# Kernel tuning notes

Hardware: AMD Instinct MI355X
Metric: run time of the kernel (lower is better)

The kernel has to match this reference:

```python
import jax, jax.numpy as jnp
import numpy as np

D = 128
H = 4
DK = D // H


def _spmm(row, col, val, x, n):
    # sparse.mm(adj, x) with adj in COO form: out[row] += val * x[col]
    return jax.ops.segment_sum(val[:, None] * x[col], row, num_segments=n)


def _arrg(h, a1_w, a1_b, a2_w, a2_b):
    return jax.nn.leaky_relu(h @ a1_w + a1_b, negative_slope=0.01) @ a2_w + a2_b


def _cross_attn(x, q_x, q_w, k_w, v_w):
    n, d = x.shape
    m = q_x.shape[0]
    q = (q_x @ q_w).reshape(m, H, DK).transpose(1, 0, 2)   # [H, Q, dk]
    k = (x @ k_w).reshape(n, H, DK).transpose(1, 0, 2)     # [H, N, dk]
    v = (q_x @ v_w).reshape(m, H, DK).transpose(1, 0, 2)   # [H, Q, dk]
    s = jnp.einsum('hnd,hqd->hnq', k, q) / jnp.sqrt(jnp.float32(DK))
    w = jax.nn.softmax(s, axis=-1)                          # softmax over queries
    out = jnp.einsum('hnq,hqd->hnd', w, v).transpose(1, 0, 2).reshape(n, d)
    return out + x


def setup_inputs() -> dict:
    key = jax.random.key(0)
    ks = iter(jax.random.split(key, 64))
    nrm = lambda shape, s=0.05: jax.random.normal(next(ks), shape, jnp.float32) * s
    inp = {}
    inp['trans_w'] = nrm((1, D)); inp['trans_b'] = nrm((D,))
    inp['g_w'] = nrm((D, D));     inp['g_b'] = nrm((D,))
    inp['qg_w'] = nrm((D, D));    inp['qg_b'] = nrm((D,))
    inp['q_w'] = nrm((D, D)); inp['k_w'] = nrm((D, D)); inp['v_w'] = nrm((D, D))
    inp['a1_w'] = nrm((D, 2 * D)); inp['a1_b'] = nrm((2 * D,))
    inp['a2_w'] = nrm((2 * D, D)); inp['a2_b'] = nrm((D,))
    inp['x0'] = jax.random.normal(next(ks), (25000,), jnp.float32)
    inp['q0'] = jax.random.normal(next(ks), (100,), jnp.float32)
    for i in (1, 2, 3):
        inp[f'xin{i}'] = jax.random.normal(next(ks), (25000,), jnp.float32)
        inp[f'qin{i}'] = jax.random.normal(next(ks), (100,), jnp.float32)
    n_sizes = {1: 50000, 2: 75000, 3: 100000}
    q_sizes = {1: 200, 2: 300, 3: 400}
    for i in (1, 2, 3):
        e = 16 * n_sizes[i]
        inp[f'aval{i}'] = jax.random.uniform(next(ks), (e,), jnp.float32)
        inp[f'arow{i}'] = jax.random.randint(next(ks), (e,), 0, n_sizes[i], jnp.int64)
        inp[f'acol{i}'] = jax.random.randint(next(ks), (e,), 0, n_sizes[i], jnp.int64)
        qe = 16 * q_sizes[i]
        inp[f'qval{i}'] = jax.random.uniform(next(ks), (qe,), jnp.float32)
        inp[f'qrow{i}'] = jax.random.randint(next(ks), (qe,), 0, q_sizes[i], jnp.int64)
        inp[f'qcol{i}'] = jax.random.randint(next(ks), (qe,), 0, q_sizes[i], jnp.int64)
    return inp


def reference(trans_w, trans_b, g_w, g_b, qg_w, qg_b, q_w, k_w, v_w,
              a1_w, a1_b, a2_w, a2_b,
              x0, q0, xin1, xin2, xin3, qin1, qin2, qin3,
              aval1, aval2, aval3, qval1, qval2, qval3,
              arow1, acol1, arow2, acol2, arow3, acol3,
              qrow1, qcol1, qrow2, qcol2, qrow3, qcol3):
    trans = lambda v: v[:, None] @ trans_w + trans_b
    x = trans(x0)
    qx = trans(q0)
    steps = [
        (xin1, qin1, arow1, acol1, aval1, qrow1, qcol1, qval1, 50000, 200),
        (xin2, qin2, arow2, acol2, aval2, qrow2, qcol2, qval2, 75000, 300),
        (xin3, qin3, arow3, acol3, aval3, qrow3, qcol3, qval3, 100000, 400),
    ]
    for xin, qin, ar, ac, av, qr, qc, qv, n, m in steps:
        x = jnp.concatenate([x, trans(xin)], axis=0)
        qx = jnp.concatenate([qx, trans(qin)], axis=0)
        x = _spmm(ar, ac, av, x @ g_w + g_b, n)
        qx = _spmm(qr, qc, qv, qx @ qg_w + qg_b, m)
        x = _arrg(x, a1_w, a1_b, a2_w, a2_b)
        qx = _arrg(qx, a1_w, a1_b, a2_w, a2_b)
        x = _cross_attn(x, qx, q_w, k_w, v_w)
    return (x, qx)
```

## Files before the change

kernel.cpp:

```cpp
#include <hip/hip_runtime.h>

typedef unsigned short u16;
typedef __attribute__((ext_vector_type(8))) short bf16x8;
typedef __attribute__((ext_vector_type(4))) float f32x4;
typedef __attribute__((ext_vector_type(2))) unsigned u32x2;

__device__ __forceinline__ float b2f(u16 v) {
    return __uint_as_float(((unsigned)v) << 16);
}
__device__ __forceinline__ u16 f2b(float x) {
    unsigned u = __float_as_uint(x);
    unsigned r = u + 0x7FFFu + ((u >> 16) & 1u);
    return (u16)(r >> 16);
}
__device__ __forceinline__ float4 load_bf4(const u16* p) {
    ushort4 q = *(const ushort4*)p;
    float4 f;
    f.x = b2f(q.x); f.y = b2f(q.y); f.z = b2f(q.z); f.w = b2f(q.w);
    return f;
}
__device__ __forceinline__ float4 in4(const void* p, long off, bool bf) {
    if (bf) return load_bf4((const u16*)p + off);
    return *(const float4*)((const float*)p + off);
}
__device__ __forceinline__ float in1(const void* p, long off, bool bf) {
    if (bf) return b2f(((const u16*)p)[off]);
    return ((const float*)p)[off];
}
__device__ __forceinline__ int inIdx(const void* p, long i, bool i64) {
    return ((const int*)p)[i64 ? 2 * i : i];
}

__global__ void sniff_kernel(const u16* __restrict__ x0bits, const int* __restrict__ arow,
                             int* __restrict__ flags) {
    if (threadIdx.x != 0 || blockIdx.x != 0) return;
    int plaus = 0;
    for (int i = 0; i < 256; ++i) {
        u16 v = x0bits[i];
        int e = (v >> 7) & 0xFF;
        if (v == 0 || (e >= 100 && e <= 135)) plaus++;
    }
    flags[0] = (plaus >= 200) ? 1 : 0;
    int nz = 0;
    for (int i = 1; i < 128; i += 2) nz += (arow[i] != 0);
    flags[1] = (nz == 0) ? 1 : 0;
}

__global__ void trans_kernel(const void* __restrict__ v, const void* __restrict__ tw,
                             const void* __restrict__ tb, float* __restrict__ out,
                             int rows, const int* __restrict__ flags) {
    const bool bf = flags[0] != 0;
    int t = blockIdx.x * blockDim.x + threadIdx.x;
    int c4 = (t & 31) * 4;
    int r = t >> 5;
    if (r >= rows) return;
    float vv = in1(v, r, bf);
    float4 w4 = in4(tw, c4, bf);
    float4 b4 = in4(tb, c4, bf);
    float4 o;
    o.x = vv * w4.x + b4.x; o.y = vv * w4.y + b4.y;
    o.z = vv * w4.z + b4.z; o.w = vv * w4.w + b4.w;
    *(float4*)(out + (size_t)r * 128 + c4) = o;
}

__global__ void wprep_kernel(const void* __restrict__ src, u16* __restrict__ dst,
                             int K, int N, const int* __restrict__ flags) {
    const bool bf = flags[0] != 0;
    int idx = blockIdx.x * blockDim.x + threadIdx.x;
    if (idx >= K * N) return;
    int j = idx & 7, lane = (idx >> 3) & 63, t = idx >> 9;
    int KC = K >> 5;
    int kc = t % KC, ct = t / KC;
    int k = kc * 32 + (lane >> 4) * 8 + j;
    int nn = ct * 16 + (lane & 15);
    dst[idx] = f2b(in1(src, (long)k * N + nn, bf));
}

template<int KTOT, int NOUT, bool LEAKY, typename AT, typename CT>
__launch_bounds__(256)
__global__ void gemm_mfma_kernel(const AT* __restrict__ A, const u16* __restrict__ Wf,
                                 const void* __restrict__ bias, CT* __restrict__ C,
                                 int n, const int* __restrict__ flags) {
    constexpr int KC = KTOT / 32;
    constexpr int NT = NOUT / 16;
    __shared__ u16 wlds[KTOT * NOUT];
    {
        const int4* srcw = (const int4*)Wf;
        int4* dstw = (int4*)wlds;
        constexpr int NV = KTOT * NOUT * 2 / 16;
#pragma unroll
        for (int i = 0; i < NV / 256; ++i)
            dstw[i * 256 + threadIdx.x] = srcw[i * 256 + threadIdx.x];
    }
    __syncthreads();
    const bool bf = flags[0] != 0;
    const int lane = threadIdx.x & 63;
    const int wave = threadIdx.x >> 6;
    const int quad = lane >> 4, col = lane & 15;
    const int rbase = (blockIdx.x * 4 + wave) * 16;
    if (rbase >= n) return;
    int node = rbase + col; if (node >= n) node = n - 1;
    f32x4 acc[NT];
#pragma unroll
    for (int ct = 0; ct < NT; ++ct) acc[ct] = (f32x4){0.f, 0.f, 0.f, 0.f};
#pragma unroll
    for (int kc = 0; kc < KC; ++kc) {
        bf16x8 af;
        if constexpr (sizeof(AT) == 2) {
            af = *(const bf16x8*)((const u16*)A + (size_t)node * KTOT + kc * 32 + quad * 8);
        } else {
            const float* ap = (const float*)A + (size_t)node * KTOT + kc * 32 + quad * 8;
            float4 a0 = *(const float4*)ap;
            float4 a1 = *(const float4*)(ap + 4);
            af[0] = (short)f2b(a0.x); af[1] = (short)f2b(a0.y);
            af[2] = (short)f2b(a0.z); af[3] = (short)f2b(a0.w);
            af[4] = (short)f2b(a1.x); af[5] = (short)f2b(a1.y);
            af[6] = (short)f2b(a1.z); af[7] = (short)f2b(a1.w);
        }
#pragma unroll
        for (int ct = 0; ct < NT; ++ct) {
            bf16x8 wf = *(const bf16x8*)(wlds + (((ct * KC + kc) * 64 + lane) * 8));
            acc[ct] = __builtin_amdgcn_mfma_f32_16x16x32_bf16(af, wf, acc[ct], 0, 0, 0);
        }
    }
#pragma unroll
    for (int ct = 0; ct < NT; ++ct) {
        int colg = ct * 16 + col;
        float b = bias ? in1(bias, colg, bf) : 0.f;
#pragma unroll
        for (int r = 0; r < 4; ++r) {
            int row = rbase + quad * 4 + r;
            if (row >= n) continue;
            float v = acc[ct][r] + b;
            if (LEAKY) v = v > 0.f ? v : 0.01f * v;
            if constexpr (sizeof(CT) == 2) C[(size_t)row * NOUT + colg] = (CT)f2b(v);
            else                           C[(size_t)row * NOUT + colg] = (CT)v;
        }
    }
}

__launch_bounds__(256)
__global__ void gemm_qv_kernel(const float* __restrict__ A, const u16* __restrict__ Wfq,
                               const u16* __restrict__ Wfv, float* __restrict__ Cq,
                               float* __restrict__ Cv, int n) {
    __shared__ u16 wldsq[128 * 128];
    __shared__ u16 wldsv[128 * 128];
    {
        const int4* sq = (const int4*)Wfq;
        const int4* sv = (const int4*)Wfv;
        int4* dq = (int4*)wldsq;
        int4* dv = (int4*)wldsv;
#pragma unroll
        for (int i = 0; i < 8; ++i) {
            dq[i * 256 + threadIdx.x] = sq[i * 256 + threadIdx.x];
            dv[i * 256 + threadIdx.x] = sv[i * 256 + threadIdx.x];
        }
    }
    __syncthreads();
    const int lane = threadIdx.x & 63;
    const int wave = threadIdx.x >> 6;
    const int quad = lane >> 4, col = lane & 15;
    const int rbase = (blockIdx.x * 4 + wave) * 16;
    if (rbase >= n) return;
    int node = rbase + col; if (node >= n) node = n - 1;
    f32x4 accq[8], accv[8];
#pragma unroll
    for (int ct = 0; ct < 8; ++ct) {
        accq[ct] = (f32x4){0.f, 0.f, 0.f, 0.f};
        accv[ct] = (f32x4){0.f, 0.f, 0.f, 0.f};
    }
#pragma unroll
    for (int kc = 0; kc < 4; ++kc) {
        const float* ap = A + (size_t)node * 128 + kc * 32 + quad * 8;
        float4 a0 = *(const float4*)ap;
        float4 a1 = *(const float4*)(ap + 4);
        bf16x8 af;
        af[0] = (short)f2b(a0.x); af[1] = (short)f2b(a0.y);
        af[2] = (short)f2b(a0.z); af[3] = (short)f2b(a0.w);
        af[4] = (short)f2b(a1.x); af[5] = (short)f2b(a1.y);
        af[6] = (short)f2b(a1.z); af[7] = (short)f2b(a1.w);
#pragma unroll
        for (int ct = 0; ct < 8; ++ct) {
            bf16x8 wq = *(const bf16x8*)(wldsq + (((ct * 4 + kc) * 64 + lane) * 8));
            bf16x8 wv = *(const bf16x8*)(wldsv + (((ct * 4 + kc) * 64 + lane) * 8));
            accq[ct] = __builtin_amdgcn_mfma_f32_16x16x32_bf16(af, wq, accq[ct], 0, 0, 0);
            accv[ct] = __builtin_amdgcn_mfma_f32_16x16x32_bf16(af, wv, accv[ct], 0, 0, 0);
        }
    }
#pragma unroll
    for (int ct = 0; ct < 8; ++ct) {
        int colg = ct * 16 + col;
#pragma unroll
        for (int r = 0; r < 4; ++r) {
            int row = rbase + quad * 4 + r;
            if (row >= n) continue;
            Cq[(size_t)row * 128 + colg] = accq[ct][r];
            Cv[(size_t)row * 128 + colg] = accv[ct][r];
        }
    }
}

#define RSH 8
#define NBC_MAX 512
#define EPB 4096

__global__ void zero_int_kernel(int* __restrict__ p, int n) {
    int i = blockIdx.x * blockDim.x + threadIdx.x;
    if (i < n) p[i] = 0;
}

__global__ void bhist_kernel(const void* __restrict__ rows, int e, int* __restrict__ bcnt,
                             int nbc, const int* __restrict__ flags) {
    __shared__ int hist[NBC_MAX];
    const bool i64 = flags[1] != 0;
    for (int i = threadIdx.x; i < nbc; i += 256) hist[i] = 0;
    __syncthreads();
    int base = blockIdx.x * 8192;
    int end = base + 8192; if (end > e) end = e;
    for (int i = base + threadIdx.x; i < end; i += 256)
        atomicAdd(&hist[inIdx(rows, i, i64) >> RSH], 1);
    __syncthreads();
    for (int i = threadIdx.x; i < nbc; i += 256) {
        int c = hist[i];
        if (c) atomicAdd(&bcnt[i], c);
    }
}

__global__ void scanF_kernel(const int* __restrict__ bcnt, int nbc,
                             int* __restrict__ optr, int* __restrict__ ocur) {
    __shared__ int sc[NBC_MAX];
    const int tid = threadIdx.x;
    int v0 = (tid < nbc) ? bcnt[tid] : 0;
    int v1 = (tid + 256 < nbc) ? bcnt[tid + 256] : 0;
    sc[tid] = v0; sc[tid + 256] = v1;
    __syncthreads();
    for (int off = 1; off < NBC_MAX; off <<= 1) {
        int a = (tid >= off) ? sc[tid - off] : 0;
        int b = sc[tid + 256 - off];
        __syncthreads();
        sc[tid] += a;
        sc[tid + 256] += b;
        __syncthreads();
    }
    if (tid < nbc)       { int x = sc[tid] - v0;       optr[tid] = x;       ocur[tid] = x; }
    if (tid + 256 < nbc) { int x = sc[tid + 256] - v1; optr[tid + 256] = x; ocur[tid + 256] = x; }
}

__launch_bounds__(256)
__global__ void qbuild_kernel(const void* __restrict__ rows, const void* __restrict__ colsin,
                              const void* __restrict__ valsin, int e, int nrows,
                              int2* __restrict__ pack1, int* __restrict__ rowptr,
                              int* __restrict__ rowend, const int* __restrict__ flags) {
    __shared__ int hist[512], cur[512], sc[512];
    const bool bf = flags[0] != 0;
    const bool i64 = flags[1] != 0;
    const int tid = threadIdx.x;
    for (int i = tid; i < 512; i += 256) hist[i] = 0;
    __syncthreads();
    for (int i = tid; i < e; i += 256)
        atomicAdd(&hist[inIdx(rows, i, i64)], 1);
    __syncthreads();
    int v0 = hist[tid], v1 = hist[tid + 256];
    sc[tid] = v0; sc[tid + 256] = v1;
    __syncthreads();
    for (int off = 1; off < 512; off <<= 1) {
        int a = (tid >= off) ? sc[tid - off] : 0;
        int b = sc[tid + 256 - off];
        __syncthreads();
        sc[tid] += a;
        sc[tid + 256] += b;
        __syncthreads();
    }
    {
        int x = sc[tid] - v0;
        cur[tid] = x;
        if (tid < nrows) { rowptr[tid] = x; rowend[tid] = x + v0; }
        int x1 = sc[tid + 256] - v1;
        cur[tid + 256] = x1;
        if (tid + 256 < nrows) { rowptr[tid + 256] = x1; rowend[tid + 256] = x1 + v1; }
    }
    __syncthreads();
    for (int i = tid; i < e; i += 256) {
        int r = inIdx(rows, i, i64);
        int p = atomicAdd(&cur[r], 1);
        pack1[p] = (int2){inIdx(colsin, i, i64), __float_as_int(in1(valsin, i, bf))};
    }
}

__launch_bounds__(256)
__global__ void psort_kernel(const void* __restrict__ rows, const void* __restrict__ colsin,
                             const void* __restrict__ valsin, int e,
                             int* __restrict__ gcur, int2* __restrict__ pack0,
                             int nbc, const int* __restrict__ flags) {
    __shared__ int hist[NBC_MAX];
    __shared__ int scan[NBC_MAX];
    __shared__ int base[NBC_MAX];
    __shared__ int cur[NBC_MAX];
    __shared__ int2 stage[EPB];
    __shared__ u16 binof[EPB];
    const bool bf = flags[0] != 0;
    const bool i64 = flags[1] != 0;
    const int tid = threadIdx.x;
    const long s0 = (long)blockIdx.x * EPB;
    int cnt_e = e - (int)s0; if (cnt_e > EPB) cnt_e = EPB;

    for (int i = tid; i < NBC_MAX; i += 256) hist[i] = 0;
    __syncthreads();
    for (int j = tid; j < cnt_e; j += 256)
        atomicAdd(&hist[inIdx(rows, s0 + j, i64) >> RSH], 1);
    __syncthreads();
    for (int i = tid; i < NBC_MAX; i += 256) scan[i] = hist[i];
    __syncthreads();
    for (int off = 1; off < NBC_MAX; off <<= 1) {
        int a = (tid >= off) ? scan[tid - off] : 0;
        int c = scan[tid + 256 - off];
        __syncthreads();
        scan[tid] += a;
        scan[tid + 256] += c;
        __syncthreads();
    }
    for (int i = tid; i < nbc; i += 256) {
        int h = hist[i];
        cur[i] = scan[i] - h;
        base[i] = h ? atomicAdd(&gcur[i], h) : 0;
    }
    __syncthreads();
    for (int j = tid; j < cnt_e; j += 256) {
        int r = inIdx(rows, s0 + j, i64);
        int bin = r >> RSH;
        int p = atomicAdd(&cur[bin], 1);
        int2 pk;
        pk.x = ((r & ((1 << RSH) - 1)) << 20) | inIdx(colsin, s0 + j, i64);
        pk.y = __float_as_int(in1(valsin, s0 + j, bf));
        stage[p] = pk;
        binof[p] = (u16)bin;
    }
    __syncthreads();
    for (int j = tid; j < cnt_e; j += 256) {
        int bin = binof[j];
        int st = scan[bin] - hist[bin];
        pack0[base[bin] + (j - st)] = stage[j];
    }
}

__launch_bounds__(256)
__global__ void breorder256_kernel(const int2* __restrict__ pack0, const int* __restrict__ bptr,
                                   const int* __restrict__ bend, int2* __restrict__ pack1,
                                   int* __restrict__ rowptr, int* __restrict__ rowend, int n) {
    __shared__ int hist[256], scan[256], cur[256];
    const int b = blockIdx.x;
    const int s = bptr[b], e = bend[b];
    const int tid = threadIdx.x;
    hist[tid] = 0;
    __syncthreads();
    for (int i = s + tid; i < e; i += 256)
        atomicAdd(&hist[(unsigned)pack0[i].x >> 20], 1);
    __syncthreads();
    scan[tid] = hist[tid];
    __syncthreads();
    for (int off = 1; off < 256; off <<= 1) {
        int a = (tid >= off) ? scan[tid - off] : 0;
        __syncthreads();
        scan[tid] += a;
        __syncthreads();
    }
    int st = s + scan[tid] - hist[tid];
    cur[tid] = st;
    int rg = (b << RSH) + tid;
    if (rg < n) { rowptr[rg] = st; rowend[rg] = st + hist[tid]; }
    __syncthreads();
    for (int i = s + tid; i < e; i += 256) {
        int2 pk = pack0[i];
        int rl = (unsigned)pk.x >> 20;
        int p = atomicAdd(&cur[rl], 1);
        pack1[p] = (int2){pk.x & 0xFFFFF, pk.y};
    }
}

__device__ __forceinline__ void bffma8(float v, uint4 h, float* a) {
    a[0] += v * __uint_as_float(h.x << 16);
    a[1] += v * __uint_as_float(h.x & 0xFFFF0000u);
    a[2] += v * __uint_as_float(h.y << 16);
    a[3] += v * __uint_as_float(h.y & 0xFFFF0000u);
    a[4] += v * __uint_as_float(h.z << 16);
    a[5] += v * __uint_as_float(h.z & 0xFFFF0000u);
    a[6] += v * __uint_as_float(h.w << 16);
    a[7] += v * __uint_as_float(h.w & 0xFFFF0000u);
}
__global__ void spmm_kernel(const u16* __restrict__ H, const int* __restrict__ rowptr,
                            const int* __restrict__ rowend, const int2* __restrict__ pack,
                            u16* __restrict__ out, int n) {
    int w = threadIdx.x >> 6;
    int lane = threadIdx.x & 63;
    int r = blockIdx.x * 4 + w;
    if (r >= n) return;
    const int s16 = lane >> 4;
    const int l16 = lane & 15;
    int s = rowptr[r], e = rowend[r];
    float a[8] = {0.f, 0.f, 0.f, 0.f, 0.f, 0.f, 0.f, 0.f};
    int i = s + s16;
    for (; i + 12 < e; i += 16) {
        int2 p0 = pack[i], p1 = pack[i + 4], p2 = pack[i + 8], p3 = pack[i + 12];
        uint4 h0 = *(const uint4*)(H + (size_t)p0.x * 128 + l16 * 8);
        uint4 h1 = *(const uint4*)(H + (size_t)p1.x * 128 + l16 * 8);
        uint4 h2 = *(const uint4*)(H + (size_t)p2.x * 128 + l16 * 8);
        uint4 h3 = *(const uint4*)(H + (size_t)p3.x * 128 + l16 * 8);
        bffma8(__int_as_float(p0.y), h0, a);
        bffma8(__int_as_float(p1.y), h1, a);
        bffma8(__int_as_float(p2.y), h2, a);
        bffma8(__int_as_float(p3.y), h3, a);
    }
    for (; i < e; i += 4) {
        int2 p0 = pack[i];
        uint4 h0 = *(const uint4*)(H + (size_t)p0.x * 128 + l16 * 8);
        bffma8(__int_as_float(p0.y), h0, a);
    }
#pragma unroll
    for (int k = 0; k < 8; ++k) {
        a[k] += __shfl_xor(a[k], 16, 64);
        a[k] += __shfl_xor(a[k], 32, 64);
    }
    if (s16 == 0) {
        uint4 o;
        o.x = (unsigned)f2b(a[0]) | ((unsigned)f2b(a[1]) << 16);
        o.y = (unsigned)f2b(a[2]) | ((unsigned)f2b(a[3]) << 16);
        o.z = (unsigned)f2b(a[4]) | ((unsigned)f2b(a[5]) << 16);
        o.w = (unsigned)f2b(a[6]) | ((unsigned)f2b(a[7]) << 16);
        *(uint4*)(out + (size_t)r * 128 + l16 * 8) = o;
    }
}

__global__ void attn_prep_kernel(const float* __restrict__ Qq, const float* __restrict__ Qv,
                                 u16* __restrict__ Qf, u16* __restrict__ Vf,
                                 int m, int mt32) {
    int idx = blockIdx.x * blockDim.x + threadIdx.x;
    int total = 4 * mt32 * 1024;
    if (idx >= total) return;
    const int mt16 = mt32 * 2;
    const float scale = 0.17677669529663687f * 1.44269504088896340736f;
    {
        int j = idx & 7, lane = (idx >> 3) & 63;
        int t = idx >> 9;
        int h = t / mt16, qt = t - h * mt16;
        int dim = ((lane >> 4) & 3) * 8 + j;
        int query = qt * 16 + (lane & 15);
        Qf[idx] = (query < m) ? f2b(Qq[(size_t)query * 128 + h * 32 + dim] * scale) : (u16)0;
    }
    {
        int j = idx & 7, lane = (idx >> 3) & 63;
        int u = idx >> 9;
        int dh = u & 1, t = u >> 1;
        int h = t / mt32, qc = t - h * mt32;
        int query = qc * 32 + ((lane >> 4) & 3) * 8 + j;
        int dim = dh * 16 + (lane & 15);
        Vf[idx] = (query < m) ? f2b(Qv[(size_t)query * 128 + h * 32 + dim]) : (u16)0;
    }
}

__launch_bounds__(256)
__global__ void attn_mfma_kernel(const u16* __restrict__ Kb, const u16* __restrict__ Qf,
                                 const u16* __restrict__ Vf, float* __restrict__ X,
                                 int n, int m, int mt32, int pad) {
    __shared__ __align__(128) u16 Pbuf_all[4 * 1024];
    const int h = blockIdx.y;
    const int wave = threadIdx.x >> 6;
    const int lane = threadIdx.x & 63;
    const int nb = (blockIdx.x * 4 + wave) * 32;
    if (nb >= n) return;
    const int quad = lane >> 4, col = lane & 15;
    int node0 = nb + col;      if (node0 >= n) node0 = n - 1;
    int node1 = nb + 16 + col; if (node1 >= n) node1 = n - 1;
    bf16x8 kf0 = *(const bf16x8*)(Kb + (size_t)node0 * 128 + h * 32 + quad * 8);
    bf16x8 kf1 = *(const bf16x8*)(Kb + (size_t)node1 * 128 + h * 32 + quad * 8);
    f32x4 O00 = {0.f, 0.f, 0.f, 0.f}, O01 = {0.f, 0.f, 0.f, 0.f};
    f32x4 O10 = {0.f, 0.f, 0.f, 0.f}, O11 = {0.f, 0.f, 0.f, 0.f};
    const f32x4 zero = {0.f, 0.f, 0.f, 0.f};
    float Lp0[4] = {0.f, 0.f, 0.f, 0.f};
    float Lp1[4] = {0.f, 0.f, 0.f, 0.f};
    u16* Pw0 = Pbuf_all + wave * 1024;
    u16* Pw1 = Pw0 + 512;
    uint2* pw0[2]; uint2* pw1[2];
    pw0[0] = (uint2*)(Pw0 + col * 16 + quad * 4);
    pw0[1] = (uint2*)(Pw0 + 256 + col * 16 + quad * 4);
    pw1[0] = (uint2*)(Pw1 + col * 16 + quad * 4);
    pw1[1] = (uint2*)(Pw1 + 256 + col * 16 + quad * 4);
    const unsigned paddr0 = (unsigned)(uintptr_t)Pw0 + (unsigned)(quad * 256 + col * 8);
    const unsigned paddr1 = (unsigned)(uintptr_t)Pw1 + (unsigned)(quad * 256 + col * 8);
    const u16* Qbase = Qf + (size_t)h * (mt32 * 2) * 512;
    const u16* Vbase = Vf + (size_t)h * mt32 * 1024;
    for (int qc = 0; qc < mt32; ++qc) {
#pragma unroll
        for (int half = 0; half < 2; ++half) {
            bf16x8 qfr = *(const bf16x8*)(Qbase + (size_t)(qc * 2 + half) * 512 + lane * 8);
            f32x4 S0 = __builtin_amdgcn_mfma_f32_16x16x32_bf16(kf0, qfr, zero, 0, 0, 0);
            f32x4 S1 = __builtin_amdgcn_mfma_f32_16x16x32_bf16(kf1, qfr, zero, 0, 0, 0);
            float a0 = __builtin_amdgcn_exp2f(fminf(S0[0], 115.f));
            float a1 = __builtin_amdgcn_exp2f(fminf(S0[1], 115.f));
            float a2 = __builtin_amdgcn_exp2f(fminf(S0[2], 115.f));
            float a3 = __builtin_amdgcn_exp2f(fminf(S0[3], 115.f));
            float b0 = __builtin_amdgcn_exp2f(fminf(S1[0], 115.f));
            float b1 = __builtin_amdgcn_exp2f(fminf(S1[1], 115.f));
            float b2 = __builtin_amdgcn_exp2f(fminf(S1[2], 115.f));
            float b3 = __builtin_amdgcn_exp2f(fminf(S1[3], 115.f));
            Lp0[0] += a0; Lp0[1] += a1; Lp0[2] += a2; Lp0[3] += a3;
            Lp1[0] += b0; Lp1[1] += b1; Lp1[2] += b2; Lp1[3] += b3;
            unsigned ra, rb, rc, rd;
            asm volatile("v_cvt_pk_bf16_f32 %0, %1, %2" : "=v"(ra) : "v"(a0), "v"(a1));
            asm volatile("v_cvt_pk_bf16_f32 %0, %1, %2" : "=v"(rb) : "v"(a2), "v"(a3));
            asm volatile("v_cvt_pk_bf16_f32 %0, %1, %2" : "=v"(rc) : "v"(b0), "v"(b1));
            asm volatile("v_cvt_pk_bf16_f32 %0, %1, %2" : "=v"(rd) : "v"(b2), "v"(b3));
            uint2 pka; pka.x = ra; pka.y = rb;
            uint2 pkb; pkb.x = rc; pkb.y = rd;
            *pw0[half] = pka;
            *pw1[half] = pkb;
        }
        asm volatile("s_waitcnt lgkmcnt(0)" ::: "memory");
        u32x2 t0a, t0b, t1a, t1b;
        asm volatile("ds_read_b64_tr_b16 %0, %1" : "=&v"(t0a) : "v"(paddr0) : "memory");
        asm volatile("ds_read_b64_tr_b16 %0, %1 offset:128" : "=&v"(t0b) : "v"(paddr0) : "memory");
        asm volatile("ds_read_b64_tr_b16 %0, %1" : "=&v"(t1a) : "v"(paddr1) : "memory");
        asm volatile("ds_read_b64_tr_b16 %0, %1 offset:128" : "=&v"(t1b) : "v"(paddr1) : "memory");
        asm volatile("s_waitcnt lgkmcnt(0)" ::: "memory");
        __builtin_amdgcn_sched_barrier(0);
        bf16x8 pf0, pf1;
        ((u32x2*)&pf0)[0] = t0a; ((u32x2*)&pf0)[1] = t0b;
        ((u32x2*)&pf1)[0] = t1a; ((u32x2*)&pf1)[1] = t1b;
        bf16x8 v0 = *(const bf16x8*)(Vbase + (size_t)(qc * 2 + 0) * 512 + lane * 8);
        bf16x8 v1 = *(const bf16x8*)(Vbase + (size_t)(qc * 2 + 1) * 512 + lane * 8);
        O00 = __builtin_amdgcn_mfma_f32_16x16x32_bf16(pf0, v0, O00, 0, 0, 0);
        O01 = __builtin_amdgcn_mfma_f32_16x16x32_bf16(pf0, v1, O01, 0, 0, 0);
        O10 = __builtin_amdgcn_mfma_f32_16x16x32_bf16(pf1, v0, O10, 0, 0, 0);
        O11 = __builtin_amdgcn_mfma_f32_16x16x32_bf16(pf1, v1, O11, 0, 0, 0);
    }
#pragma unroll
    for (int mask = 1; mask < 16; mask <<= 1) {
#pragma unroll
        for (int r = 0; r < 4; ++r) {
            Lp0[r] += __shfl_xor(Lp0[r], mask, 64);
            Lp1[r] += __shfl_xor(Lp1[r], mask, 64);
        }
    }
#pragma unroll
    for (int r = 0; r < 4; ++r) {
        int nd = nb + quad * 4 + r;
        if (nd < n) {
            float inv = 1.f / fmaxf(Lp0[r] - (float)pad, 1e-35f);
            float* xp = X + (size_t)nd * 128 + h * 32;
            xp[col]      += O00[r] * inv;
            xp[16 + col] += O01[r] * inv;
        }
        int nd1 = nb + 16 + quad * 4 + r;
        if (nd1 < n) {
            float inv = 1.f / fmaxf(Lp1[r] - (float)pad, 1e-35f);
            float* xp = X + (size_t)nd1 * 128 + h * 32;
            xp[col]      += O10[r] * inv;
            xp[16 + col] += O11[r] * inv;
        }
    }
}

__global__ void out_writer_kernel(const float* __restrict__ in, void* __restrict__ out,
                                  long elem_off, int n4, const int* __restrict__ flags) {
    const bool bf = flags[0] != 0;
    int i = blockIdx.x * blockDim.x + threadIdx.x;
    if (i >= n4) return;
    float4 v = ((const float4*)in)[i];
    if (bf) {
        ushort4 q; q.x = f2b(v.x); q.y = f2b(v.y); q.z = f2b(v.z); q.w = f2b(v.w);
        ((ushort4*)((u16*)out + elem_off))[i] = q;
    } else {
        ((float4*)((float*)out + elem_off))[i] = v;
    }
}

extern "C" void kernel_launch(void* const* d_in, const int* in_sizes, int n_in,
                              void* d_out, int out_size, void* d_ws, size_t ws_size,
                              hipStream_t stream) {
    (void)n_in; (void)out_size; (void)ws_size;
    const void* trans_w = d_in[0];
    const void* trans_b = d_in[1];
    const void* g_w  = d_in[2];
    const void* g_b  = d_in[3];
    const void* qg_w = d_in[4];
    const void* qg_b = d_in[5];
    const void* q_w  = d_in[6];
    const void* k_w  = d_in[7];
    const void* v_w  = d_in[8];
    const void* a1_w = d_in[9];
    const void* a1_b = d_in[10];
    const void* a2_w = d_in[11];
    const void* a2_b = d_in[12];
    const void* x0   = d_in[13];
    const void* q0   = d_in[14];

    int ixin[3], iqin[3], iaval[3], iarow[3], iacol[3], iqval[3], iqrow[3], iqcol[3];
    if (in_sizes[16] == 100) {
        for (int s = 0; s < 3; ++s) {
            ixin[s] = 15 + 2 * s; iqin[s] = 16 + 2 * s;
            int b = 21 + 6 * s;
            iaval[s] = b; iarow[s] = b + 1; iacol[s] = b + 2;
            iqval[s] = b + 3; iqrow[s] = b + 4; iqcol[s] = b + 5;
        }
    } else {
        int xs[3] = {15,16,17}, qs_[3] = {18,19,20};
        int av[3] = {21,22,23}, qv[3] = {24,25,26};
        int ar[3] = {27,29,31}, ac[3] = {28,30,32};
        int qr[3] = {33,35,37}, qc[3] = {34,36,38};
        for (int s = 0; s < 3; ++s) {
            ixin[s]=xs[s]; iqin[s]=qs_[s]; iaval[s]=av[s]; iqval[s]=qv[s];
            iarow[s]=ar[s]; iacol[s]=ac[s]; iqrow[s]=qr[s]; iqcol[s]=qc[s];
        }
    }

    char* p = (char*)d_ws;
    auto alloc = [&](size_t bytes) -> char* {
        char* r = p;
        p += (bytes + 255) & ~(size_t)255;
        return r;
    };
    int*   flags = (int*)alloc(256);
    const int NMAX = 100000;
    float* X   = (float*)alloc((size_t)NMAX * 128 * 4);
    u16*   T1b = (u16*)  alloc((size_t)NMAX * 128 * 2);
    u16*   Xs  = (u16*)  alloc((size_t)NMAX * 128 * 2);
    u16*   T2  = (u16*)  alloc((size_t)NMAX * 256 * 2);
    float* QX  = (float*)alloc((size_t)400 * 128 * 4);
    u16*   QT1b= (u16*)  alloc((size_t)400 * 128 * 2);
    u16*   QXs = (u16*)  alloc((size_t)400 * 128 * 2);
    u16*   QT2 = (u16*)  alloc((size_t)400 * 256 * 2);
    float* Qq  = (float*)alloc((size_t)400 * 128 * 4);
    float* Qv  = (float*)alloc((size_t)400 * 128 * 4);
    u16*   Qfrag = (u16*)alloc((size_t)4 * 13 * 1024 * 2);
    u16*   Vfrag = (u16*)alloc((size_t)4 * 13 * 1024 * 2);
    u16* Wg  = (u16*)alloc((size_t)128 * 128 * 2);
    u16* Wqg = (u16*)alloc((size_t)128 * 128 * 2);
    u16* Wa1 = (u16*)alloc((size_t)128 * 256 * 2);
    u16* Wa2 = (u16*)alloc((size_t)256 * 128 * 2);
    u16* Wk  = (u16*)alloc((size_t)128 * 128 * 2);
    u16* Wq  = (u16*)alloc((size_t)128 * 128 * 2);
    u16* Wv  = (u16*)alloc((size_t)128 * 128 * 2);
    int2*  csr_pack = (int2*)alloc((size_t)1600000 * 8);
    int*   bcnt   = (int*)alloc((size_t)NBC_MAX * 4);
    int*   bktptr = (int*)alloc((size_t)NBC_MAX * 4);
    int*   bktcur = (int*)alloc((size_t)NBC_MAX * 4);
    int*   rowptr = (int*)alloc((size_t)NMAX * 4);
    int*   rowend = (int*)alloc((size_t)NMAX * 4);
    int2*  pack0  = (int2*)T2;

    sniff_kernel<<<1, 64, 0, stream>>>((const u16*)x0, (const int*)d_in[iarow[0]], flags);

    auto wprep = [&](const void* src, u16* dst, int K, int N) {
        wprep_kernel<<<(K * N + 255) / 256, 256, 0, stream>>>(src, dst, K, N, flags);
    };
    wprep(g_w,  Wg,  128, 128);
    wprep(qg_w, Wqg, 128, 128);
    wprep(a1_w, Wa1, 128, 256);
    wprep(a2_w, Wa2, 256, 128);
    wprep(k_w,  Wk,  128, 128);
    wprep(q_w,  Wq,  128, 128);
    wprep(v_w,  Wv,  128, 128);

    auto launch_trans = [&](const void* v, float* out, int rows) {
        trans_kernel<<<(rows * 32 + 255) / 256, 256, 0, stream>>>(v, trans_w, trans_b, out, rows, flags);
    };
    auto build_spmm = [&](const void* rows, const void* colsidx, const void* vals, int e,
                          int nrows, const u16* H, u16* OUT) {
        if (nrows <= 512) {
            qbuild_kernel<<<1, 256, 0, stream>>>(rows, colsidx, vals, e, nrows,
                                                 csr_pack, rowptr, rowend, flags);
        } else {
            int nbc = (nrows + 255) >> RSH;
            zero_int_kernel<<<(nbc + 255) / 256, 256, 0, stream>>>(bcnt, nbc);
            bhist_kernel<<<(e + 8191) / 8192, 256, 0, stream>>>(rows, e, bcnt, nbc, flags);
            scanF_kernel<<<1, 256, 0, stream>>>(bcnt, nbc, bktptr, bktcur);
            psort_kernel<<<(e + EPB - 1) / EPB, 256, 0, stream>>>(rows, colsidx, vals, e,
                                                                  bktcur, pack0, nbc, flags);
            breorder256_kernel<<<nbc, 256, 0, stream>>>(pack0, bktptr, bktcur, csr_pack,
                                                        rowptr, rowend, nrows);
        }
        spmm_kernel<<<(nrows + 3) / 4, 256, 0, stream>>>(H, rowptr, rowend, csr_pack,
                                                         OUT, nrows);
    };

    int nprev = in_sizes[13];
    int mprev = in_sizes[14];
    launch_trans(x0, X, nprev);
    launch_trans(q0, QX, mprev);

    const int ns[3] = {50000, 75000, 100000};
    const int ms[3] = {200, 300, 400};
    for (int s = 0; s < 3; ++s) {
        const int n = ns[s], m = ms[s];
        const int e  = in_sizes[iaval[s]];
        const int qe = in_sizes[iqval[s]];
        launch_trans(d_in[ixin[s]], X + (size_t)nprev * 128, n - nprev);
        launch_trans(d_in[iqin[s]], QX + (size_t)mprev * 128, m - mprev);
        const int gb  = (n + 63) / 64;
        const int gqb = (m + 63) / 64;
        gemm_mfma_kernel<128, 128, false, float, u16><<<gb, 256, 0, stream>>>(X, Wg, g_b, T1b, n, flags);
        build_spmm(d_in[iarow[s]], d_in[iacol[s]], d_in[iaval[s]], e, n, T1b, Xs);
        gemm_mfma_kernel<128, 128, false, float, u16><<<gqb, 256, 0, stream>>>(QX, Wqg, qg_b, QT1b, m, flags);
        build_spmm(d_in[iqrow[s]], d_in[iqcol[s]], d_in[iqval[s]], qe, m, QT1b, QXs);
        gemm_mfma_kernel<128, 256, true, u16, u16><<<gb, 256, 0, stream>>>(Xs, Wa1, a1_b, T2, n, flags);
        gemm_mfma_kernel<256, 128, false, u16, float><<<gb, 256, 0, stream>>>(T2, Wa2, a2_b, X, n, flags);
        gemm_mfma_kernel<128, 256, true, u16, u16><<<gqb, 256, 0, stream>>>(QXs, Wa1, a1_b, QT2, m, flags);
        gemm_mfma_kernel<256, 128, false, u16, float><<<gqb, 256, 0, stream>>>(QT2, Wa2, a2_b, QX, m, flags);
        gemm_mfma_kernel<128, 128, false, float, u16><<<gb, 256, 0, stream>>>(X, Wk, nullptr, T1b, n, flags);
        gemm_qv_kernel<<<gqb, 256, 0, stream>>>(QX, Wq, Wv, Qq, Qv, m);
        const int mt32 = (m + 31) / 32;
        const int pad = mt32 * 32 - m;
        const int ptot = 4 * mt32 * 1024;
        attn_prep_kernel<<<(ptot + 255) / 256, 256, 0, stream>>>(Qq, Qv, Qfrag, Vfrag, m, mt32);
        attn_mfma_kernel<<<dim3((n + 127) / 128, 4), 256, 0, stream>>>(T1b, Qfrag, Vfrag, X, n, m, mt32, pad);
        nprev = n;
        mprev = m;
    }

    const int n4x = 100000 * 128 / 4;
    const int n4q = 400 * 128 / 4;
    out_writer_kernel<<<(n4x + 255) / 256, 256, 0, stream>>>(X, d_out, 0, n4x, flags);
    out_writer_kernel<<<(n4q + 255) / 256, 256, 0, stream>>>(QX, d_out, (long)100000 * 128, n4q, flags);
}
```

Measured before the change: 1.218 ms.

## Software-pipeline attention loop with double-buffered LDS P tiles

Restructures the per-wave attention loop so the S=K·Q MFMA, exp and P-store for chunk qc overlap with the transposed LDS reads and PV MFMA of chunk qc-1. It uses two LDS buffers per wave, preloads V fragments one iteration ahead, and waits with a partial lgkmcnt. This is meant to hide LDS round-trip latency and waitcnt stalls in the inner loop. In exchange LDS use doubles, register pressure rises, and correctness now depends on the lgkmcnt(4) ordering.

```diff
diff --git a/kernel.cpp b/kernel.cpp
--- a/kernel.cpp
+++ b/kernel.cpp
@@ -461,7 +461,7 @@
 __global__ void attn_mfma_kernel(const u16* __restrict__ Kb, const u16* __restrict__ Qf,
                                  const u16* __restrict__ Vf, float* __restrict__ X,
                                  int n, int m, int mt32, int pad) {
-    __shared__ __align__(128) u16 Pbuf_all[4 * 1024];
+    __shared__ __align__(128) u16 Pbuf_all[4 * 2048];
     const int h = blockIdx.y;
     const int wave = threadIdx.x >> 6;
     const int lane = threadIdx.x & 63;
@@ -477,18 +477,14 @@
     const f32x4 zero = {0.f, 0.f, 0.f, 0.f};
     float Lp0[4] = {0.f, 0.f, 0.f, 0.f};
     float Lp1[4] = {0.f, 0.f, 0.f, 0.f};
-    u16* Pw0 = Pbuf_all + wave * 1024;
-    u16* Pw1 = Pw0 + 512;
-    uint2* pw0[2]; uint2* pw1[2];
-    pw0[0] = (uint2*)(Pw0 + col * 16 + quad * 4);
-    pw0[1] = (uint2*)(Pw0 + 256 + col * 16 + quad * 4);
-    pw1[0] = (uint2*)(Pw1 + col * 16 + quad * 4);
-    pw1[1] = (uint2*)(Pw1 + 256 + col * 16 + quad * 4);
-    const unsigned paddr0 = (unsigned)(uintptr_t)Pw0 + (unsigned)(quad * 256 + col * 8);
-    const unsigned paddr1 = (unsigned)(uintptr_t)Pw1 + (unsigned)(quad * 256 + col * 8);
+    u16* bufA = Pbuf_all + wave * 2048;
+    u16* bufB = bufA + 1024;
+    const unsigned wslot = (unsigned)(col * 16 + quad * 4);
+    const unsigned rslot = (unsigned)(quad * 256 + col * 8);
     const u16* Qbase = Qf + (size_t)h * (mt32 * 2) * 512;
     const u16* Vbase = Vf + (size_t)h * mt32 * 1024;
-    for (int qc = 0; qc < mt32; ++qc) {
+
+    auto computeS = [&](int qc, u16* buf) {
 #pragma unroll
         for (int half = 0; half < 2; ++half) {
             bf16x8 qfr = *(const bf16x8*)(Qbase + (size_t)(qc * 2 + half) * 512 + lane * 8);
@@ -511,26 +507,57 @@
             asm volatile("v_cvt_pk_bf16_f32 %0, %1, %2" : "=v"(rd) : "v"(b2), "v"(b3));
             uint2 pka; pka.x = ra; pka.y = rb;
             uint2 pkb; pkb.x = rc; pkb.y = rd;
-            *pw0[half] = pka;
-            *pw1[half] = pkb;
-        }
+            *(uint2*)(buf + half * 256 + wslot) = pka;
+            *(uint2*)(buf + 512 + half * 256 + wslot) = pkb;
+        }
+    };
+
+    computeS(0, bufA);
+    bf16x8 v0p = *(const bf16x8*)(Vbase + 0 * 512 + lane * 8);
+    bf16x8 v1p = *(const bf16x8*)(Vbase + 1 * 512 + lane * 8);
+    u16* bprev = bufA;
+    u16* bcur = bufB;
+    for (int qc = 1; qc < mt32; ++qc) {
         asm volatile("s_waitcnt lgkmcnt(0)" ::: "memory");
+        unsigned pa0 = (unsigned)(uintptr_t)bprev + rslot;
+        unsigned pa1 = pa0 + 1024;
         u32x2 t0a, t0b, t1a, t1b;
-        asm volatile("ds_read_b64_tr_b16 %0, %1" : "=&v"(t0a) : "v"(paddr0) : "memory");
-        asm volatile("ds_read_b64_tr_b16 %0, %1 offset:128" : "=&v"(t0b) : "v"(paddr0) : "memory");
-        asm volatile("ds_read_b64_tr_b16 %0, %1" : "=&v"(t1a) : "v"(paddr1) : "memory");
-        asm volatile("ds_read_b64_tr_b16 %0, %1 offset:128" : "=&v"(t1b) : "v"(paddr1) : "memory");
+        asm volatile("ds_read_b64_tr_b16 %0, %1" : "=&v"(t0a) : "v"(pa0) : "memory");
+        asm volatile("ds_read_b64_tr_b16 %0, %1 offset:128" : "=&v"(t0b) : "v"(pa0) : "memory");
+        asm volatile("ds_read_b64_tr_b16 %0, %1" : "=&v"(t1a) : "v"(pa1) : "memory");
+        asm volatile("ds_read_b64_tr_b16 %0, %1 offset:128" : "=&v"(t1b) : "v"(pa1) : "memory");
+        computeS(qc, bcur);
+        asm volatile("s_waitcnt lgkmcnt(4)" ::: "memory");
+        __builtin_amdgcn_sched_barrier(0);
+        bf16x8 pf0, pf1;
+        ((u32x2*)&pf0)[0] = t0a; ((u32x2*)&pf0)[1] = t0b;
+        ((u32x2*)&pf1)[0] = t1a; ((u32x2*)&pf1)[1] = t1b;
+        O00 = __builtin_amdgcn_mfma_f32_16x16x32_bf16(pf0, v0p, O00, 0, 0, 0);
+        O01 = __builtin_amdgcn_mfma_f32_16x16x32_bf16(pf0, v1p, O01, 0, 0, 0);
+        O10 = __builtin_amdgcn_mfma_f32_16x16x32_bf16(pf1, v0p, O10, 0, 0, 0);
+        O11 = __builtin_amdgcn_mfma_f32_16x16x32_bf16(pf1, v1p, O11, 0, 0, 0);
+        v0p = *(const bf16x8*)(Vbase + (size_t)(qc * 2 + 0) * 512 + lane * 8);
+        v1p = *(const bf16x8*)(Vbase + (size_t)(qc * 2 + 1) * 512 + lane * 8);
+        u16* t = bprev; bprev = bcur; bcur = t;
+    }
+    {
+        asm volatile("s_waitcnt lgkmcnt(0)" ::: "memory");
+        unsigned pa0 = (unsigned)(uintptr_t)bprev + rslot;
+        unsigned pa1 = pa0 + 1024;
+        u32x2 t0a, t0b, t1a, t1b;
+        asm volatile("ds_read_b64_tr_b16 %0, %1" : "=&v"(t0a) : "v"(pa0) : "memory");
+        asm volatile("ds_read_b64_tr_b16 %0, %1 offset:128" : "=&v"(t0b) : "v"(pa0) : "memory");
+        asm volatile("ds_read_b64_tr_b16 %0, %1" : "=&v"(t1a) : "v"(pa1) : "memory");
+        asm volatile("ds_read_b64_tr_b16 %0, %1 offset:128" : "=&v"(t1b) : "v"(pa1) : "memory");
         asm volatile("s_waitcnt lgkmcnt(0)" ::: "memory");
         __builtin_amdgcn_sched_barrier(0);
         bf16x8 pf0, pf1;
         ((u32x2*)&pf0)[0] = t0a; ((u32x2*)&pf0)[1] = t0b;
         ((u32x2*)&pf1)[0] = t1a; ((u32x2*)&pf1)[1] = t1b;
-        bf16x8 v0 = *(const bf16x8*)(Vbase + (size_t)(qc * 2 + 0) * 512 + lane * 8);
-        bf16x8 v1 = *(const bf16x8*)(Vbase + (size_t)(qc * 2 + 1) * 512 + lane * 8);
-        O00 = __builtin_amdgcn_mfma_f32_16x16x32_bf16(pf0, v0, O00, 0, 0, 0);
-        O01 = __builtin_amdgcn_mfma_f32_16x16x32_bf16(pf0, v1, O01, 0, 0, 0);
-        O10 = __builtin_amdgcn_mfma_f32_16x16x32_bf16(pf1, v0, O10, 0, 0, 0);
-        O11 = __builtin_amdgcn_mfma_f32_16x16x32_bf16(pf1, v1, O11, 0, 0, 0);
+        O00 = __builtin_amdgcn_mfma_f32_16x16x32_bf16(pf0, v0p, O00, 0, 0, 0);
+        O01 = __builtin_amdgcn_mfma_f32_16x16x32_bf16(pf0, v1p, O01, 0, 0, 0);
+        O10 = __builtin_amdgcn_mfma_f32_16x16x32_bf16(pf1, v0p, O10, 0, 0, 0);
+        O11 = __builtin_amdgcn_mfma_f32_16x16x32_bf16(pf1, v1p, O11, 0, 0, 0);
     }
 #pragma unroll
     for (int mask = 1; mask < 16; mask <<= 1) {
```

Measured after the change: 1.223 ms. Within noise of the previous version (+0.5%).
